# Kernel tuning notes

Hardware: AMD Instinct MI355X
Metric: run time of the kernel (lower is better)

Reference implementation:

```python
import jax, jax.numpy as jnp
import numpy as np

EPS = 1e-5  # torch BatchNorm1d default

def _batchnorm(h, g, b):
    # training-mode BN over batch axis, biased variance (matches torch)
    mu = h.mean(axis=0)
    var = ((h - mu) ** 2).mean(axis=0)
    return g * (h - mu) / jnp.sqrt(var + EPS) + b


def setup_inputs() -> dict:
    key = jax.random.key(0)
    ks = jax.random.split(key, 8)
    B = 65536
    x = jax.random.normal(ks[0], (B, 784), dtype=jnp.float32)
    W0 = jax.random.normal(ks[1], (10, 784), dtype=jnp.float32) * (1.0 / np.sqrt(784))
    b0 = jax.random.normal(ks[2], (10,), dtype=jnp.float32) * 0.01
    g0 = jnp.ones((10,), dtype=jnp.float32)
    beta0 = jnp.zeros((10,), dtype=jnp.float32)
    Ws = jax.random.normal(ks[3], (62, 10, 10), dtype=jnp.float32) * (1.0 / np.sqrt(10))
    bs = jax.random.normal(ks[4], (62, 10), dtype=jnp.float32) * 0.01
    gs = jnp.ones((62, 10), dtype=jnp.float32)
    betas = jnp.zeros((62, 10), dtype=jnp.float32)
    Wf = jax.random.normal(ks[5], (10, 10), dtype=jnp.float32) * (1.0 / np.sqrt(10))
    bf = jax.random.normal(ks[6], (10,), dtype=jnp.float32) * 0.01
    return {"x": x, "W0": W0, "b0": b0, "g0": g0, "beta0": beta0,
            "Ws": Ws, "bs": bs, "gs": gs, "betas": betas, "Wf": Wf, "bf": bf}


def reference(x, W0, b0, g0, beta0, Ws, bs, gs, betas, Wf, bf):
    # Linear(784->10) + BN
    h = x @ W0.T + b0                     # [B,10]
    h = _batchnorm(h, g0, beta0)
    def step(h, layer):
        W, b, g, beta = layer
        h = h @ W.T + b
        h = _batchnorm(h, g, beta)
        return h, None
    h, _ = jax.lax.scan(step, h, (Ws, bs, gs, betas))
    # final Linear(10,10), no BN
    return h @ Wf.T + bf
```

## Files before the change

kernel.cpp:

```cpp
#include <hip/hip_runtime.h>

#define B_ROWS 65536
#define D_IN 784
#define NF 10
#define NLAYERS 62
#define TILE_COLS 28
#define NTILES 28
#define BLOCK_A 64
#define GRID_A 1024
#define PAD_COLS 30
#define NSTAT 65
#define QLOADS 7

__global__ __launch_bounds__(BLOCK_A) void passA(const float* __restrict__ x,
                                                 const float* __restrict__ W0,
                                                 const float* __restrict__ b0,
                                                 float* __restrict__ zout,
                                                 float* __restrict__ partials) {
  __shared__ float xs[BLOCK_A][PAD_COLS];
  const int tid = threadIdx.x;
  const int rowbase = blockIdx.x * BLOCK_A;
  const float* xblk = x + (size_t)rowbase * D_IN;

  int goff[QLOADS], doff[QLOADS];
#pragma unroll
  for (int q = 0; q < QLOADS; ++q) {
    int g = tid + q * BLOCK_A;
    int row = g / 7, pos = g % 7;
    goff[q] = row * D_IN + pos * 4;
    doff[q] = row * PAD_COLS + pos * 4;
  }
  float* xsf = &xs[0][0];

  float acc[NF];
#pragma unroll
  for (int j = 0; j < NF; ++j) acc[j] = b0[j];

  float4 p[QLOADS];
#pragma unroll
  for (int q = 0; q < QLOADS; ++q)
    p[q] = *reinterpret_cast<const float4*>(xblk + goff[q]);
#pragma unroll
  for (int q = 0; q < QLOADS; ++q) {
    float2* dst = reinterpret_cast<float2*>(xsf + doff[q]);
    dst[0] = make_float2(p[q].x, p[q].y);
    dst[1] = make_float2(p[q].z, p[q].w);
  }

  for (int t = 0; t < NTILES; ++t) {
    __syncthreads();
    if (t + 1 < NTILES) {
      const float* src = xblk + (t + 1) * TILE_COLS;
#pragma unroll
      for (int q = 0; q < QLOADS; ++q)
        p[q] = *reinterpret_cast<const float4*>(src + goff[q]);
    }
    const int k0 = t * TILE_COLS;
    float xv[TILE_COLS];
#pragma unroll
    for (int i = 0; i < TILE_COLS; i += 2) {
      float2 v = *reinterpret_cast<const float2*>(&xs[tid][i]);
      xv[i] = v.x; xv[i + 1] = v.y;
    }
#pragma unroll
    for (int i = 0; i < TILE_COLS; ++i) {
#pragma unroll
      for (int j = 0; j < NF; ++j)
        acc[j] = fmaf(xv[i], W0[j * D_IN + k0 + i], acc[j]);
    }
    __syncthreads();
    if (t + 1 < NTILES) {
#pragma unroll
      for (int q = 0; q < QLOADS; ++q) {
        float2* dst = reinterpret_cast<float2*>(xsf + doff[q]);
        dst[0] = make_float2(p[q].x, p[q].y);
        dst[1] = make_float2(p[q].z, p[q].w);
      }
    }
  }

  float* zr = zout + (size_t)(rowbase + tid) * NF;
#pragma unroll
  for (int j = 0; j < NF; j += 2)
    *reinterpret_cast<float2*>(zr + j) = make_float2(acc[j], acc[j + 1]);

  float vals[NSTAT];
  {
    int v = 0;
#pragma unroll
    for (int j = 0; j < NF; ++j) vals[v++] = acc[j];
#pragma unroll
    for (int i = 0; i < NF; ++i)
#pragma unroll
      for (int j = i; j < NF; ++j) vals[v++] = acc[i] * acc[j];
  }
#pragma unroll
  for (int k = 0; k < NSTAT; ++k) {
    float s = vals[k];
#pragma unroll
    for (int m = 1; m < 64; m <<= 1) s += __shfl_xor(s, m, 64);
    if (tid == (k & 63)) partials[blockIdx.x * NSTAT + k] = s;
  }
}

__global__ __launch_bounds__(512) void passB(const float* __restrict__ partials,
                                             const float* __restrict__ g0,
                                             const float* __restrict__ beta0,
                                             const float* __restrict__ Ws,
                                             const float* __restrict__ bs,
                                             const float* __restrict__ gs,
                                             const float* __restrict__ betas,
                                             const float* __restrict__ Wf,
                                             const float* __restrict__ bf,
                                             float* __restrict__ statsf) {
  __shared__ double S[NSTAT], Sp[4][NSTAT];
  __shared__ double M[NF][NF], Cov[NF][NF], P[NF][NF], T[NF][NF], Cz[NF][NF];
  __shared__ double cvec[NF], meanv[NF], muz[NF], czv[NF], sv[NF], tv[NF], mu0[NF];
  __shared__ float Wl[NLAYERS * 100];
  __shared__ float bl[NLAYERS * NF], gl[NLAYERS * NF], bel[NLAYERS * NF];
  const int tid = threadIdx.x;

  for (int i = tid; i < NLAYERS * 100; i += 512) Wl[i] = Ws[i];
  for (int i = tid; i < NLAYERS * NF; i += 512) {
    bl[i] = bs[i]; gl[i] = gs[i]; bel[i] = betas[i];
  }

  if (tid < 4 * NSTAT) {
    const int part = tid / NSTAT, k = tid - part * NSTAT;
    double s = 0.0;
    const int b0i = part * (GRID_A / 4);
#pragma unroll 4
    for (int b = 0; b < GRID_A / 4; ++b) s += (double)partials[(b0i + b) * NSTAT + k];
    Sp[part][k] = s;
  }
  __syncthreads();
  if (tid < NSTAT) S[tid] = Sp[0][tid] + Sp[1][tid] + Sp[2][tid] + Sp[3][tid];
  __syncthreads();

  if (tid < NF) mu0[tid] = S[tid] / (double)B_ROWS;
  __syncthreads();
  if (tid < 100) {
    int i = tid / 10, j = tid % 10;
    int a = i < j ? i : j, b2 = i < j ? j : i;
    int idx = 10 + 10 * a - (a * (a - 1)) / 2 + (b2 - a);
    Cov[i][j] = S[idx] / (double)B_ROWS - mu0[i] * mu0[j];
  }
  __syncthreads();
  if (tid < NF) {
    double s0 = (double)g0[tid] / sqrt(Cov[tid][tid] + 1e-5);
    sv[tid] = s0;
    cvec[tid] = (double)beta0[tid] - s0 * mu0[tid];
    meanv[tid] = (double)beta0[tid];
  }
  __syncthreads();
  if (tid < 100) {
    int i = tid / 10, j = tid % 10;
    M[i][j] = (i == j) ? sv[j] : 0.0;
    Cov[i][j] = Cov[i][j] * sv[i] * sv[j];
  }
  __syncthreads();

  for (int k = 0; k < NLAYERS; ++k) {
    const float* W = &Wl[k * 100];
    const float* bb = &bl[k * NF];
    const float* gg = &gl[k * NF];
    const float* be = &bel[k * NF];
    if (tid < 100) {
      int i = tid / 10, j = tid % 10;
      double t1 = 0.0, t2 = 0.0;
#pragma unroll
      for (int l = 0; l < 10; ++l) {
        t1 += (double)W[i * 10 + l] * Cov[l][j];
        t2 += M[i][l] * (double)W[j * 10 + l];
      }
      T[i][j] = t1; P[i][j] = t2;
    }
    if (tid >= 128 && tid < 138) {
      int j = tid - 128;
      double m1 = (double)bb[j], c1 = (double)bb[j];
#pragma unroll
      for (int l = 0; l < 10; ++l) {
        m1 += meanv[l] * (double)W[j * 10 + l];
        c1 += cvec[l] * (double)W[j * 10 + l];
      }
      muz[j] = m1; czv[j] = c1;
    }
    __syncthreads();
    if (tid < 100) {
      int i = tid / 10, j = tid % 10;
      double t3 = 0.0;
#pragma unroll
      for (int l = 0; l < 10; ++l) t3 += T[i][l] * (double)W[j * 10 + l];
      Cz[i][j] = t3;
    }
    __syncthreads();
    if (tid < NF) {
      double s = (double)gg[tid] / sqrt(Cz[tid][tid] + 1e-5);
      sv[tid] = s;
      tv[tid] = (double)be[tid] - s * muz[tid];
    }
    __syncthreads();
    if (tid < 100) {
      int i = tid / 10, j = tid % 10;
      M[i][j] = P[i][j] * sv[j];
      Cov[i][j] = Cz[i][j] * sv[i] * sv[j];
    }
    if (tid >= 128 && tid < 138) {
      int j = tid - 128;
      cvec[j] = czv[j] * sv[j] + tv[j];
      meanv[j] = (double)be[j];
    }
    __syncthreads();
  }

  if (tid < 100) {
    int i = tid / 10, j = tid % 10;
    double t2 = 0.0;
#pragma unroll
    for (int l = 0; l < 10; ++l) t2 += M[i][l] * (double)Wf[j * 10 + l];
    P[i][j] = t2;
  }
  if (tid >= 128 && tid < 138) {
    int j = tid - 128;
    double c1 = (double)bf[j];
#pragma unroll
    for (int l = 0; l < 10; ++l) c1 += cvec[l] * (double)Wf[j * 10 + l];
    czv[j] = c1;
  }
  __syncthreads();
  if (tid < 100) statsf[tid] = (float)P[tid / 10][tid % 10];
  if (tid >= 128 && tid < 138) statsf[100 + (tid - 128)] = (float)czv[tid - 128];
}

__global__ __launch_bounds__(256) void passC(float* __restrict__ z_inout,
                                             const float* __restrict__ statsf) {
  const int r = blockIdx.x * 256 + threadIdx.x;
  float* pz = z_inout + (size_t)r * NF;
  float zr[NF];
#pragma unroll
  for (int j = 0; j < NF; j += 2) {
    float2 v = *reinterpret_cast<const float2*>(pz + j);
    zr[j] = v.x; zr[j + 1] = v.y;
  }
  float acc[NF];
#pragma unroll
  for (int j = 0; j < NF; ++j) acc[j] = statsf[100 + j];
#pragma unroll
  for (int l = 0; l < NF; ++l)
#pragma unroll
    for (int j = 0; j < NF; ++j)
      acc[j] = fmaf(zr[l], statsf[l * 10 + j], acc[j]);
#pragma unroll
  for (int j = 0; j < NF; j += 2)
    *reinterpret_cast<float2*>(pz + j) = make_float2(acc[j], acc[j + 1]);
}

extern "C" void kernel_launch(void* const* d_in, const int* in_sizes, int n_in,
                              void* d_out, int out_size, void* d_ws, size_t ws_size,
                              hipStream_t stream) {
  const float* x     = (const float*)d_in[0];
  const float* W0    = (const float*)d_in[1];
  const float* b0    = (const float*)d_in[2];
  const float* g0    = (const float*)d_in[3];
  const float* beta0 = (const float*)d_in[4];
  const float* Ws    = (const float*)d_in[5];
  const float* bs    = (const float*)d_in[6];
  const float* gs    = (const float*)d_in[7];
  const float* betas = (const float*)d_in[8];
  const float* Wf    = (const float*)d_in[9];
  const float* bf    = (const float*)d_in[10];
  float* out = (float*)d_out;

  float* partials = (float*)d_ws;
  float* statsf   = (float*)d_ws + GRID_A * NSTAT;

  passA<<<GRID_A, BLOCK_A, 0, stream>>>(x, W0, b0, out, partials);
  passB<<<1, 512, 0, stream>>>(partials, g0, beta0, Ws, bs, gs, betas, Wf, bf, statsf);
  passC<<<256, 256, 0, stream>>>(out, statsf);
}
```

Baseline: 477.8 us.

## Split K across waves in passA and shrink passB to one float wavefront

passA now uses 256 threads per block, with each of four waves handling a quarter of the 784-wide reduction for the same 64 rows. Each wave loads x directly into registers with double-buffered float4 loads instead of staging through shared memory, and the partial sums are combined through LDS. The statistics reduction is split across the waves and stored transposed. passB becomes a single 64-thread wavefront doing the 62-layer covariance propagation in fp32 registers with few barriers, and it drops bias/beta terms that cancel under BN. This risks lower precision than the previous double-precision path.

Result: slower. 561.3 us (+17.5%).

```diff
diff --git a/kernel.cpp b/kernel.cpp
--- a/kernel.cpp
+++ b/kernel.cpp
@@ -1,235 +1,235 @@
 #include <hip/hip_runtime.h>
 
-#define B_ROWS 65536
-#define D_IN 784
-#define NF 10
-#define NLAYERS 62
-#define TILE_COLS 28
-#define NTILES 28
-#define BLOCK_A 64
-#define GRID_A 1024
-#define PAD_COLS 30
+#define NROWS 65536
+#define DIN   784
+#define NF    10
+#define NL    62
 #define NSTAT 65
-#define QLOADS 7
-
-__global__ __launch_bounds__(BLOCK_A) void passA(const float* __restrict__ x,
-                                                 const float* __restrict__ W0,
-                                                 const float* __restrict__ b0,
-                                                 float* __restrict__ zout,
-                                                 float* __restrict__ partials) {
-  __shared__ float xs[BLOCK_A][PAD_COLS];
+#define NB    1024
+#define ROWS_PB 64
+#define KCH   196
+
+#define STATSF_OFF_B 0
+#define PART_OFF_B   512
+
+#define ELT(v,c) ((c)==0?(v).x:((c)==1?(v).y:((c)==2?(v).z:(v).w)))
+
+__global__ __launch_bounds__(256, 4) void passA(const float* __restrict__ x,
+                                                const float* __restrict__ W0,
+                                                const float* __restrict__ b0,
+                                                float* __restrict__ zout,
+                                                float* __restrict__ partials) {
+  __shared__ float comb[4][ROWS_PB][NF];
   const int tid = threadIdx.x;
-  const int rowbase = blockIdx.x * BLOCK_A;
-  const float* xblk = x + (size_t)rowbase * D_IN;
-
-  int goff[QLOADS], doff[QLOADS];
-#pragma unroll
-  for (int q = 0; q < QLOADS; ++q) {
-    int g = tid + q * BLOCK_A;
-    int row = g / 7, pos = g % 7;
-    goff[q] = row * D_IN + pos * 4;
-    doff[q] = row * PAD_COLS + pos * 4;
-  }
-  float* xsf = &xs[0][0];
+  const int lane = tid & 63;
+  const int wv = __builtin_amdgcn_readfirstlane(tid >> 6);
+
+  const int rowbase = blockIdx.x * ROWS_PB;
+  const int row = rowbase + lane;
+  const float* xr = x + (size_t)row * DIN + wv * KCH;
+  const float* wp = W0 + wv * KCH;
 
   float acc[NF];
 #pragma unroll
-  for (int j = 0; j < NF; ++j) acc[j] = b0[j];
-
-  float4 p[QLOADS];
-#pragma unroll
-  for (int q = 0; q < QLOADS; ++q)
-    p[q] = *reinterpret_cast<const float4*>(xblk + goff[q]);
-#pragma unroll
-  for (int q = 0; q < QLOADS; ++q) {
-    float2* dst = reinterpret_cast<float2*>(xsf + doff[q]);
-    dst[0] = make_float2(p[q].x, p[q].y);
-    dst[1] = make_float2(p[q].z, p[q].w);
-  }
-
-  for (int t = 0; t < NTILES; ++t) {
-    __syncthreads();
-    if (t + 1 < NTILES) {
-      const float* src = xblk + (t + 1) * TILE_COLS;
-#pragma unroll
-      for (int q = 0; q < QLOADS; ++q)
-        p[q] = *reinterpret_cast<const float4*>(src + goff[q]);
-    }
-    const int k0 = t * TILE_COLS;
-    float xv[TILE_COLS];
-#pragma unroll
-    for (int i = 0; i < TILE_COLS; i += 2) {
-      float2 v = *reinterpret_cast<const float2*>(&xs[tid][i]);
-      xv[i] = v.x; xv[i + 1] = v.y;
-    }
-#pragma unroll
-    for (int i = 0; i < TILE_COLS; ++i) {
-#pragma unroll
-      for (int j = 0; j < NF; ++j)
-        acc[j] = fmaf(xv[i], W0[j * D_IN + k0 + i], acc[j]);
-    }
-    __syncthreads();
-    if (t + 1 < NTILES) {
-#pragma unroll
-      for (int q = 0; q < QLOADS; ++q) {
-        float2* dst = reinterpret_cast<float2*>(xsf + doff[q]);
-        dst[0] = make_float2(p[q].x, p[q].y);
-        dst[1] = make_float2(p[q].z, p[q].w);
-      }
-    }
-  }
-
-  float* zr = zout + (size_t)(rowbase + tid) * NF;
-#pragma unroll
-  for (int j = 0; j < NF; j += 2)
-    *reinterpret_cast<float2*>(zr + j) = make_float2(acc[j], acc[j + 1]);
+  for (int j = 0; j < NF; ++j) acc[j] = (wv == 0) ? b0[j] : 0.f;
+
+  float4 Aq[7], Bq[7];
+#pragma unroll
+  for (int q = 0; q < 7; ++q) Aq[q] = *(const float4*)(xr + q * 4);
+
+#define BATCH(bi, CUR, NXT)                                                    \
+  do {                                                                         \
+    if ((bi) < 6) {                                                            \
+      _Pragma("unroll") for (int q = 0; q < 7; ++q)                            \
+          NXT[q] = *(const float4*)(xr + ((bi) + 1) * 28 + q * 4);             \
+    }                                                                          \
+    _Pragma("unroll") for (int e = 0; e < 28; ++e) {                           \
+      float xv = ELT(CUR[(e) >> 2], (e)&3);                                    \
+      _Pragma("unroll") for (int j = 0; j < NF; ++j)                           \
+          acc[j] = fmaf(xv, wp[j * DIN + (bi)*28 + e], acc[j]);                \
+    }                                                                          \
+  } while (0)
+
+  BATCH(0, Aq, Bq); BATCH(1, Bq, Aq); BATCH(2, Aq, Bq); BATCH(3, Bq, Aq);
+  BATCH(4, Aq, Bq); BATCH(5, Bq, Aq); BATCH(6, Aq, Bq);
+#undef BATCH
+
+#pragma unroll
+  for (int j = 0; j < NF; ++j) comb[wv][lane][j] = acc[j];
+  __syncthreads();
+  float a[NF];
+#pragma unroll
+  for (int j = 0; j < NF; ++j)
+    a[j] = comb[0][lane][j] + comb[1][lane][j] + comb[2][lane][j] + comb[3][lane][j];
+
+  if (wv == 0) {
+    float* zr = zout + (size_t)row * NF;
+#pragma unroll
+    for (int j = 0; j < NF; j += 2) *(float2*)(zr + j) = make_float2(a[j], a[j + 1]);
+  }
 
   float vals[NSTAT];
   {
     int v = 0;
 #pragma unroll
-    for (int j = 0; j < NF; ++j) vals[v++] = acc[j];
+    for (int j = 0; j < NF; ++j) vals[v++] = a[j];
 #pragma unroll
     for (int i = 0; i < NF; ++i)
 #pragma unroll
-      for (int j = i; j < NF; ++j) vals[v++] = acc[i] * acc[j];
-  }
+      for (int j = i; j < NF; ++j) vals[v++] = a[i] * a[j];
+  }
+  const int kb2 = wv * 17, ke2 = (wv == 3) ? NSTAT : wv * 17 + 17;
 #pragma unroll
   for (int k = 0; k < NSTAT; ++k) {
-    float s = vals[k];
-#pragma unroll
-    for (int m = 1; m < 64; m <<= 1) s += __shfl_xor(s, m, 64);
-    if (tid == (k & 63)) partials[blockIdx.x * NSTAT + k] = s;
-  }
-}
-
-__global__ __launch_bounds__(512) void passB(const float* __restrict__ partials,
-                                             const float* __restrict__ g0,
-                                             const float* __restrict__ beta0,
-                                             const float* __restrict__ Ws,
-                                             const float* __restrict__ bs,
-                                             const float* __restrict__ gs,
-                                             const float* __restrict__ betas,
-                                             const float* __restrict__ Wf,
-                                             const float* __restrict__ bf,
-                                             float* __restrict__ statsf) {
-  __shared__ double S[NSTAT], Sp[4][NSTAT];
-  __shared__ double M[NF][NF], Cov[NF][NF], P[NF][NF], T[NF][NF], Cz[NF][NF];
-  __shared__ double cvec[NF], meanv[NF], muz[NF], czv[NF], sv[NF], tv[NF], mu0[NF];
-  __shared__ float Wl[NLAYERS * 100];
-  __shared__ float bl[NLAYERS * NF], gl[NLAYERS * NF], bel[NLAYERS * NF];
-  const int tid = threadIdx.x;
-
-  for (int i = tid; i < NLAYERS * 100; i += 512) Wl[i] = Ws[i];
-  for (int i = tid; i < NLAYERS * NF; i += 512) {
-    bl[i] = bs[i]; gl[i] = gs[i]; bel[i] = betas[i];
-  }
-
-  if (tid < 4 * NSTAT) {
-    const int part = tid / NSTAT, k = tid - part * NSTAT;
-    double s = 0.0;
-    const int b0i = part * (GRID_A / 4);
-#pragma unroll 4
-    for (int b = 0; b < GRID_A / 4; ++b) s += (double)partials[(b0i + b) * NSTAT + k];
-    Sp[part][k] = s;
+    if (k >= kb2 && k < ke2) {
+      float s = vals[k];
+#pragma unroll
+      for (int m = 1; m < 64; m <<= 1) s += __shfl_xor(s, m, 64);
+      if (lane == 0) partials[k * NB + blockIdx.x] = s;
+    }
+  }
+}
+
+__global__ __launch_bounds__(64, 1) void passB(const float* __restrict__ partials,
+                                               const float* __restrict__ Ws,
+                                               const float* __restrict__ g0,
+                                               const float* __restrict__ gs,
+                                               const float* __restrict__ betas,
+                                               const float* __restrict__ Wfin,
+                                               const float* __restrict__ bfin,
+                                               float* __restrict__ statsf) {
+  __shared__ double Sd[NSTAT];
+  __shared__ float tb[2 * NF * NF];
+  __shared__ float svl[2 * NF];
+  const int lane = threadIdx.x;
+  const int il = lane < NF ? lane : NF - 1;
+  const bool owner = lane < NF;
+
+  {
+    const float* pr = partials + (size_t)lane * NB;
+    double a0 = 0, a1 = 0, a2 = 0, a3 = 0;
+    for (int b = 0; b < NB; b += 4) {
+      float4 v = *(const float4*)(pr + b);
+      a0 += v.x; a1 += v.y; a2 += v.z; a3 += v.w;
+    }
+    Sd[lane] = (a0 + a1) + (a2 + a3);
+    if (lane == 0) {
+      const float* p2 = partials + (size_t)64 * NB;
+      double c0 = 0, c1 = 0, c2 = 0, c3 = 0;
+      for (int b = 0; b < NB; b += 4) {
+        float4 v = *(const float4*)(p2 + b);
+        c0 += v.x; c1 += v.y; c2 += v.z; c3 += v.w;
+      }
+      Sd[64] = (c0 + c1) + (c2 + c3);
+    }
   }
   __syncthreads();
-  if (tid < NSTAT) S[tid] = Sp[0][tid] + Sp[1][tid] + Sp[2][tid] + Sp[3][tid];
+
+  const double invN = 1.0 / (double)NROWS;
+  double mu[NF];
+#pragma unroll
+  for (int j = 0; j < NF; ++j) mu[j] = Sd[j] * invN;
+  const double mu_own = Sd[il] * invN;
+
+  const int idxd = NF + il * NF - (il * (il - 1)) / 2;
+  double var_own = Sd[idxd] * invN - mu_own * mu_own;
+  double s_own_d = (double)g0[il] / sqrt(var_own + 1e-5);
+  if (owner) svl[NF + il] = (float)s_own_d;
   __syncthreads();
-
-  if (tid < NF) mu0[tid] = S[tid] / (double)B_ROWS;
-  __syncthreads();
-  if (tid < 100) {
-    int i = tid / 10, j = tid % 10;
-    int a = i < j ? i : j, b2 = i < j ? j : i;
-    int idx = 10 + 10 * a - (a * (a - 1)) / 2 + (b2 - a);
-    Cov[i][j] = S[idx] / (double)B_ROWS - mu0[i] * mu0[j];
-  }
-  __syncthreads();
-  if (tid < NF) {
-    double s0 = (double)g0[tid] / sqrt(Cov[tid][tid] + 1e-5);
-    sv[tid] = s0;
-    cvec[tid] = (double)beta0[tid] - s0 * mu0[tid];
-    meanv[tid] = (double)beta0[tid];
-  }
-  __syncthreads();
-  if (tid < 100) {
-    int i = tid / 10, j = tid % 10;
-    M[i][j] = (i == j) ? sv[j] : 0.0;
-    Cov[i][j] = Cov[i][j] * sv[i] * sv[j];
-  }
-  __syncthreads();
-
-  for (int k = 0; k < NLAYERS; ++k) {
-    const float* W = &Wl[k * 100];
-    const float* bb = &bl[k * NF];
-    const float* gg = &gl[k * NF];
-    const float* be = &bel[k * NF];
-    if (tid < 100) {
-      int i = tid / 10, j = tid % 10;
-      double t1 = 0.0, t2 = 0.0;
-#pragma unroll
-      for (int l = 0; l < 10; ++l) {
-        t1 += (double)W[i * 10 + l] * Cov[l][j];
-        t2 += M[i][l] * (double)W[j * 10 + l];
+  float sjf[NF];
+#pragma unroll
+  for (int j = 0; j < NF; ++j) sjf[j] = svl[NF + j];
+
+  float CovR[NF], Mrow[NF], dvv[NF];
+#pragma unroll
+  for (int j = 0; j < NF; ++j) {
+    int a_ = il < j ? il : j, b_ = il < j ? j : il;
+    int idx = NF + a_ * NF - (a_ * (a_ - 1)) / 2 + (b_ - a_);
+    double cov = Sd[idx] * invN - mu_own * mu[j];
+    CovR[j] = (float)(cov * s_own_d) * sjf[j];
+    Mrow[j] = (il == j) ? (float)s_own_d : 0.f;
+    dvv[j] = -(float)mu[j] * sjf[j];
+  }
+
+  for (int k = 0; k < NL; ++k) {
+    const float* W = Ws + k * 100;
+    const int sl = (k & 1) * NF * NF;
+    const int ssl = (k & 1) * NF;
+
+    float VR[NF];
+#pragma unroll
+    for (int l = 0; l < NF; ++l) {
+      float t = 0.f;
+#pragma unroll
+      for (int m = 0; m < NF; ++m) t = fmaf(CovR[m], W[l * 10 + m], t);
+      VR[l] = t;
+    }
+    if (owner) {
+#pragma unroll
+      for (int l = 0; l < NF; ++l) tb[sl + il * NF + l] = VR[l];
+    }
+    __syncthreads();
+    float YR[NF];
+#pragma unroll
+    for (int l = 0; l < NF; ++l) YR[l] = tb[sl + l * NF + il];
+    float CzR[NF];
+#pragma unroll
+    for (int j = 0; j < NF; ++j) {
+      float t = 0.f;
+#pragma unroll
+      for (int l = 0; l < NF; ++l) t = fmaf(YR[l], W[j * 10 + l], t);
+      CzR[j] = t;
+    }
+    float cz_own = CzR[0];
+#pragma unroll
+    for (int j = 1; j < NF; ++j) cz_own = (il == j) ? CzR[j] : cz_own;
+    float s2 = gs[k * NF + il] / sqrtf(cz_own + 1e-5f);
+    if (owner) svl[ssl + il] = s2;
+
+    float Pt[NF], Dt[NF];
+#pragma unroll
+    for (int j = 0; j < NF; ++j) {
+      float t = 0.f, u = 0.f;
+#pragma unroll
+      for (int l = 0; l < NF; ++l) {
+        t = fmaf(Mrow[l], W[j * 10 + l], t);
+        u = fmaf(dvv[l], W[j * 10 + l], u);
       }
-      T[i][j] = t1; P[i][j] = t2;
-    }
-    if (tid >= 128 && tid < 138) {
-      int j = tid - 128;
-      double m1 = (double)bb[j], c1 = (double)bb[j];
-#pragma unroll
-      for (int l = 0; l < 10; ++l) {
-        m1 += meanv[l] * (double)W[j * 10 + l];
-        c1 += cvec[l] * (double)W[j * 10 + l];
-      }
-      muz[j] = m1; czv[j] = c1;
+      Pt[j] = t; Dt[j] = u;
     }
     __syncthreads();
-    if (tid < 100) {
-      int i = tid / 10, j = tid % 10;
-      double t3 = 0.0;
-#pragma unroll
-      for (int l = 0; l < 10; ++l) t3 += T[i][l] * (double)W[j * 10 + l];
-      Cz[i][j] = t3;
-    }
-    __syncthreads();
-    if (tid < NF) {
-      double s = (double)gg[tid] / sqrt(Cz[tid][tid] + 1e-5);
-      sv[tid] = s;
-      tv[tid] = (double)be[tid] - s * muz[tid];
-    }
-    __syncthreads();
-    if (tid < 100) {
-      int i = tid / 10, j = tid % 10;
-      M[i][j] = P[i][j] * sv[j];
-      Cov[i][j] = Cz[i][j] * sv[i] * sv[j];
-    }
-    if (tid >= 128 && tid < 138) {
-      int j = tid - 128;
-      cvec[j] = czv[j] * sv[j] + tv[j];
-      meanv[j] = (double)be[j];
-    }
-    __syncthreads();
-  }
-
-  if (tid < 100) {
-    int i = tid / 10, j = tid % 10;
-    double t2 = 0.0;
-#pragma unroll
-    for (int l = 0; l < 10; ++l) t2 += M[i][l] * (double)Wf[j * 10 + l];
-    P[i][j] = t2;
-  }
-  if (tid >= 128 && tid < 138) {
-    int j = tid - 128;
-    double c1 = (double)bf[j];
-#pragma unroll
-    for (int l = 0; l < 10; ++l) c1 += cvec[l] * (double)Wf[j * 10 + l];
-    czv[j] = c1;
-  }
-  __syncthreads();
-  if (tid < 100) statsf[tid] = (float)P[tid / 10][tid % 10];
-  if (tid >= 128 && tid < 138) statsf[100 + (tid - 128)] = (float)czv[tid - 128];
+#pragma unroll
+    for (int j = 0; j < NF; ++j) sjf[j] = svl[ssl + j];
+#pragma unroll
+    for (int j = 0; j < NF; ++j) {
+      CovR[j] = CzR[j] * s2 * sjf[j];
+      Mrow[j] = Pt[j] * sjf[j];
+      dvv[j] = Dt[j] * sjf[j];
+    }
+  }
+
+  float cvecf[NF];
+#pragma unroll
+  for (int j = 0; j < NF; ++j) cvecf[j] = dvv[j] + betas[(NL - 1) * NF + j];
+  float Ff[NF], cf[NF];
+#pragma unroll
+  for (int j = 0; j < NF; ++j) {
+    float t = 0.f, u = bfin[j];
+#pragma unroll
+    for (int l = 0; l < NF; ++l) {
+      t = fmaf(Mrow[l], Wfin[j * 10 + l], t);
+      u = fmaf(cvecf[l], Wfin[j * 10 + l], u);
+    }
+    Ff[j] = t; cf[j] = u;
+  }
+  if (owner) {
+#pragma unroll
+    for (int j = 0; j < NF; ++j) statsf[il * NF + j] = Ff[j];
+  }
+  if (lane == 0) {
+#pragma unroll
+    for (int j = 0; j < NF; ++j) statsf[100 + j] = cf[j];
+  }
 }
 
 __global__ __launch_bounds__(256) void passC(float* __restrict__ z_inout,
@@ -239,20 +239,18 @@
   float zr[NF];
 #pragma unroll
   for (int j = 0; j < NF; j += 2) {
-    float2 v = *reinterpret_cast<const float2*>(pz + j);
+    float2 v = *(const float2*)(pz + j);
     zr[j] = v.x; zr[j + 1] = v.y;
   }
-  float acc[NF];
-#pragma unroll
-  for (int j = 0; j < NF; ++j) acc[j] = statsf[100 + j];
+  float acc2[NF];
+#pragma unroll
+  for (int j = 0; j < NF; ++j) acc2[j] = statsf[100 + j];
 #pragma unroll
   for (int l = 0; l < NF; ++l)
 #pragma unroll
-    for (int j = 0; j < NF; ++j)
-      acc[j] = fmaf(zr[l], statsf[l * 10 + j], acc[j]);
-#pragma unroll
-  for (int j = 0; j < NF; j += 2)
-    *reinterpret_cast<float2*>(pz + j) = make_float2(acc[j], acc[j + 1]);
+    for (int j = 0; j < NF; ++j) acc2[j] = fmaf(zr[l], statsf[l * 10 + j], acc2[j]);
+#pragma unroll
+  for (int j = 0; j < NF; j += 2) *(float2*)(pz + j) = make_float2(acc2[j], acc2[j + 1]);
 }
 
 extern "C" void kernel_launch(void* const* d_in, const int* in_sizes, int n_in,
@@ -262,19 +260,17 @@
   const float* W0    = (const float*)d_in[1];
   const float* b0    = (const float*)d_in[2];
   const float* g0    = (const float*)d_in[3];
-  const float* beta0 = (const float*)d_in[4];
   const float* Ws    = (const float*)d_in[5];
-  const float* bs    = (const float*)d_in[6];
   const float* gs    = (const float*)d_in[7];
   const float* betas = (const float*)d_in[8];
-  const float* Wf    = (const float*)d_in[9];
-  const float* bf    = (const float*)d_in[10];
+  const float* Wfin  = (const float*)d_in[9];
+  const float* bfin  = (const float*)d_in[10];
   float* out = (float*)d_out;
 
-  float* partials = (float*)d_ws;
-  float* statsf   = (float*)d_ws + GRID_A * NSTAT;
-
-  passA<<<GRID_A, BLOCK_A, 0, stream>>>(x, W0, b0, out, partials);
-  passB<<<1, 512, 0, stream>>>(partials, g0, beta0, Ws, bs, gs, betas, Wf, bf, statsf);
+  float* statsf   = (float*)((char*)d_ws + STATSF_OFF_B);
+  float* partials = (float*)((char*)d_ws + PART_OFF_B);
+
+  passA<<<NB, 256, 0, stream>>>(x, W0, b0, out, partials);
+  passB<<<1, 64, 0, stream>>>(partials, Ws, g0, gs, betas, Wfin, bfin, statsf);
   passC<<<256, 256, 0, stream>>>(out, statsf);
 }
```
